# Optimization experiments

Measured on AMD Instinct MI355X. Metric: run time of the kernel, lower is better.

## Reference

```python
import jax, jax.numpy as jnp
import numpy as np

MP = 10242  # number of coarse (pooled) vertices = L.shape[0]


def setup_inputs() -> dict:
    key = jax.random.key(0)
    k1, k2, k3, k4 = jax.random.split(key, 4)
    B, M, F = 16, 40962, 128
    NNZ = 40968  # ~4 nonzeros per coarse vertex (barycentric pooling)
    x = jax.random.normal(k1, (B, M, F), dtype=jnp.float32)
    rows = jax.random.randint(k2, (NNZ,), 0, MP, dtype=jnp.int64)
    cols = jax.random.randint(k3, (NNZ,), 0, M, dtype=jnp.int64)
    vals = jax.random.uniform(k4, (NNZ,), dtype=jnp.float32)
    return {"x": x, "rows": rows, "cols": cols, "vals": vals}


def reference(x, rows, cols, vals):
    # Equivalent of tf.sparse_tensor_dense_matmul(L, reshape(transpose(x)))
    # L: sparse [Mp, M] in COO (rows, cols, vals); x: [B, M, F].
    # out[b, p, f] = sum_{k: rows[k]==p} vals[k] * x[b, cols[k], f]
    gathered = x[:, cols, :] * vals[None, :, None]          # [B, nnz, F]
    gathered = jnp.transpose(gathered, (1, 0, 2))           # [nnz, B, F]
    pooled = jax.ops.segment_sum(gathered, rows, num_segments=MP)  # [Mp, B, F]
    return jnp.transpose(pooled, (1, 0, 2))                 # [B, Mp, F]
```

## Files before the change

### kernel.cpp

```cpp
#include <hip/hip_runtime.h>

constexpr int MP  = 10242;
constexpr int B   = 16;
constexpr int M   = 40962;
constexpr int F   = 128;
constexpr int CAP = 32;

typedef float f32x4 __attribute__((ext_vector_type(4)));

__global__ void build_ell_kernel(const int* __restrict__ rows,
                                 const int* __restrict__ cols,
                                 const float* __restrict__ vals,
                                 int* __restrict__ counts,
                                 int2* __restrict__ ell,
                                 unsigned char* __restrict__ used,
                                 int nnz) {
    int k = blockIdx.x * blockDim.x + threadIdx.x;
    if (k < nnz) {
        int p = rows[k];
        int c = cols[k];
        if (used) used[c] = 1;
        int slot = atomicAdd(&counts[p], 1);
        if (slot < CAP) {
            ell[p * CAP + slot] = make_int2(c, __float_as_int(vals[k]));
        }
    }
}

__global__ __launch_bounds__(256)
void transpose_kernel(const float4* __restrict__ x,
                      const unsigned char* __restrict__ used,
                      float4* __restrict__ xt) {
    int m = blockIdx.x * 4 + (threadIdx.x >> 6);
    if (m >= M || !used[m]) return;
    int lane = threadIdx.x & 63;
    const float4* src = x + ((size_t)(lane >> 5) * M + (size_t)m) * 32 + (lane & 31);
    float4*       dst = xt + (size_t)m * 512 + lane;
    f32x4 v[8];
#pragma unroll
    for (int i = 0; i < 8; ++i)
        v[i] = __builtin_nontemporal_load((const f32x4*)(src + (size_t)(2 * i) * M * 32));
#pragma unroll
    for (int i = 0; i < 8; ++i)
        dst[i * 64] = *(float4*)&v[i];
}

__global__ __launch_bounds__(256)
void pool_xt_kernel(const float4* __restrict__ xt,
                    const int* __restrict__ counts,
                    const int2* __restrict__ ell,
                    float4* __restrict__ out) {
    const int p = blockIdx.x;
    const int t = threadIdx.x;
    int n = counts[p];
    n = n < CAP ? n : CAP;
    const int2* pe = ell + p * CAP;

    f32x4 acc0 = {0.f, 0.f, 0.f, 0.f}, acc1 = {0.f, 0.f, 0.f, 0.f};
    int j = 0;
    for (; j + 2 <= n; j += 2) {
        int2 e0 = pe[j], e1 = pe[j + 1];
        const f32x4* r0 = (const f32x4*)(xt + (size_t)e0.x * 512);
        const f32x4* r1 = (const f32x4*)(xt + (size_t)e1.x * 512);
        f32x4 a0 = r0[t], a1 = r0[t + 256];
        f32x4 b0 = r1[t], b1 = r1[t + 256];
        float v0 = __int_as_float(e0.y), v1 = __int_as_float(e1.y);
        acc0 += v0 * a0; acc1 += v0 * a1;
        acc0 += v1 * b0; acc1 += v1 * b1;
    }
    if (j < n) {
        int2 e = pe[j];
        const f32x4* r = (const f32x4*)(xt + (size_t)e.x * 512);
        float v = __int_as_float(e.y);
        acc0 += v * r[t]; acc1 += v * r[t + 256];
    }
    int b0i = t >> 5, l = t & 31;
    f32x4* o0 = (f32x4*)(out + ((size_t)b0i * MP + p) * 32 + l);
    f32x4* o1 = (f32x4*)(out + ((size_t)(b0i + 8) * MP + p) * 32 + l);
    __builtin_nontemporal_store(acc0, o0);
    __builtin_nontemporal_store(acc1, o1);
}

__global__ __launch_bounds__(256)
void pool_direct_kernel(const float4* __restrict__ x,
                        const int* __restrict__ counts,
                        const int2* __restrict__ ell,
                        float4* __restrict__ out) {
    const int p    = blockIdx.x;
    const int q    = threadIdx.x >> 6;
    const int lane = threadIdx.x & 63;
    const int bA   = (q << 1) | (lane >> 5);
    const int bB   = bA + 8;
    const int l    = lane & 31;

    int n = counts[p];
    n = n < CAP ? n : CAP;
    const int2* pe = ell + p * CAP;
    const float4* xA = x + (size_t)bA * (M * (F / 4));
    const float4* xB = x + (size_t)bB * (M * (F / 4));

    f32x4 accA = {0.f, 0.f, 0.f, 0.f}, accB = {0.f, 0.f, 0.f, 0.f};
    for (int j = 0; j < n; ++j) {
        int2 e = pe[j];
        float v = __int_as_float(e.y);
        f32x4 a = *(const f32x4*)&xA[(size_t)e.x * 32 + l];
        f32x4 c = *(const f32x4*)&xB[(size_t)e.x * 32 + l];
        accA += v * a;
        accB += v * c;
    }
    f32x4* oA = (f32x4*)(out + ((size_t)bA * MP + p) * 32 + l);
    f32x4* oB = (f32x4*)(out + ((size_t)bB * MP + p) * 32 + l);
    __builtin_nontemporal_store(accA, oA);
    __builtin_nontemporal_store(accB, oB);
}

extern "C" void kernel_launch(void* const* d_in, const int* in_sizes, int n_in,
                              void* d_out, int out_size, void* d_ws, size_t ws_size,
                              hipStream_t stream) {
    const float* x    = (const float*)d_in[0];
    const int*   rows = (const int*)d_in[1];
    const int*   cols = (const int*)d_in[2];
    const float* vals = (const float*)d_in[3];
    float* out = (float*)d_out;
    const int nnz = in_sizes[1];
    const int nb  = (nnz + 255) / 256;

    size_t xt_bytes   = (size_t)M * B * F * sizeof(float);
    size_t counts_off = xt_bytes;
    size_t ell_off    = counts_off + (size_t)MP * sizeof(int);
    size_t used_off   = ell_off + (size_t)MP * CAP * sizeof(int2);
    size_t needed     = used_off + (size_t)M;

    if (ws_size >= needed) {
        float* xt              = (float*)d_ws;
        int*   counts          = (int*)((char*)d_ws + counts_off);
        int2*  ell             = (int2*)((char*)d_ws + ell_off);
        unsigned char* used    = (unsigned char*)((char*)d_ws + used_off);

        hipMemsetAsync(counts, 0, MP * sizeof(int), stream);
        hipMemsetAsync(used, 0, M, stream);

        build_ell_kernel<<<nb, 256, 0, stream>>>(rows, cols, vals, counts, ell,
                                                 used, nnz);
        transpose_kernel<<<(M + 3) / 4, 256, 0, stream>>>((const float4*)x, used,
                                                          (float4*)xt);
        pool_xt_kernel<<<MP, 256, 0, stream>>>((const float4*)xt, counts, ell,
                                               (float4*)out);
    } else {
        int*  counts = (int*)d_ws;
        int2* ell    = (int2*)(counts + MP);
        hipMemsetAsync(counts, 0, MP * sizeof(int), stream);
        build_ell_kernel<<<nb, 256, 0, stream>>>(rows, cols, vals, counts, ell,
                                                 (unsigned char*)nullptr, nnz);
        pool_direct_kernel<<<MP, 256, 0, stream>>>((const float4*)x, counts, ell,
                                                   (float4*)out);
    }
}
```

Baseline: 524.7 us.

## Tile transpose through shared memory for contiguous reads and merge workspace memsets

The transpose kernel now handles 8 vertices per block, loading contiguous 4 KB runs of x per batch into shared memory and then writing each used vertex's 16x128 row block to xt. The goal is longer contiguous global reads than the old per-vertex 512-byte strided loads. The workspace is reordered so counts and the used-flag array sit next to each other and can be cleared with one memset, removing a launch. The cost is shared memory use and a block barrier, and blocks with sparse used flags still fetch some partial rows.

```diff
diff --git a/kernel.cpp b/kernel.cpp
--- a/kernel.cpp
+++ b/kernel.cpp
@@ -5,6 +5,7 @@
 constexpr int M   = 40962;
 constexpr int F   = 128;
 constexpr int CAP = 32;
+constexpr int TM  = 8;
 
 typedef float f32x4 __attribute__((ext_vector_type(4)));
 
@@ -31,18 +32,46 @@
 void transpose_kernel(const float4* __restrict__ x,
                       const unsigned char* __restrict__ used,
                       float4* __restrict__ xt) {
-    int m = blockIdx.x * 4 + (threadIdx.x >> 6);
-    if (m >= M || !used[m]) return;
-    int lane = threadIdx.x & 63;
-    const float4* src = x + ((size_t)(lane >> 5) * M + (size_t)m) * 32 + (lane & 31);
-    float4*       dst = xt + (size_t)m * 512 + lane;
-    f32x4 v[8];
+    __shared__ float4 tile[TM][B][F / 4];
+    const int m0   = blockIdx.x * TM;
+    const int t    = threadIdx.x;
+    const int w    = t >> 6;
+    const int lane = t & 63;
+
+    f32x4 v[16];
 #pragma unroll
-    for (int i = 0; i < 8; ++i)
-        v[i] = __builtin_nontemporal_load((const f32x4*)(src + (size_t)(2 * i) * M * 32));
+    for (int bi = 0; bi < 4; ++bi) {
+        int b = (w << 2) | bi;
+        const f32x4* src = (const f32x4*)(x + ((size_t)b * M + m0) * 32);
 #pragma unroll
-    for (int i = 0; i < 8; ++i)
-        dst[i * 64] = *(float4*)&v[i];
+        for (int jj = 0; jj < 4; ++jj) {
+            int idx = (jj << 6) | lane;
+            int gm  = m0 + (idx >> 5);
+            f32x4 tmp = {0.f, 0.f, 0.f, 0.f};
+            if (gm < M && used[gm]) tmp = src[idx];
+            v[(bi << 2) | jj] = tmp;
+        }
+    }
+#pragma unroll
+    for (int bi = 0; bi < 4; ++bi) {
+        int b = (w << 2) | bi;
+#pragma unroll
+        for (int jj = 0; jj < 4; ++jj) {
+            int idx = (jj << 6) | lane;
+            tile[idx >> 5][b][idx & 31] = *(float4*)&v[(bi << 2) | jj];
+        }
+    }
+    __syncthreads();
+#pragma unroll
+    for (int mm = 0; mm < TM; ++mm) {
+        int gm = m0 + mm;
+        if (gm < M && used[gm]) {
+            const float4* src = &tile[mm][0][0];
+            float4* dst = xt + (size_t)gm * 512;
+            dst[t]       = src[t];
+            dst[t + 256] = src[t + 256];
+        }
+    }
 }
 
 __global__ __launch_bounds__(256)
@@ -127,23 +156,22 @@
 
     size_t xt_bytes   = (size_t)M * B * F * sizeof(float);
     size_t counts_off = xt_bytes;
-    size_t ell_off    = counts_off + (size_t)MP * sizeof(int);
-    size_t used_off   = ell_off + (size_t)MP * CAP * sizeof(int2);
-    size_t needed     = used_off + (size_t)M;
+    size_t used_off   = counts_off + (size_t)MP * sizeof(int);
+    size_t ell_off    = (used_off + (size_t)M + 7) & ~(size_t)7;
+    size_t needed     = ell_off + (size_t)MP * CAP * sizeof(int2);
 
     if (ws_size >= needed) {
-        float* xt              = (float*)d_ws;
-        int*   counts          = (int*)((char*)d_ws + counts_off);
-        int2*  ell             = (int2*)((char*)d_ws + ell_off);
-        unsigned char* used    = (unsigned char*)((char*)d_ws + used_off);
+        float*         xt     = (float*)d_ws;
+        int*           counts = (int*)((char*)d_ws + counts_off);
+        unsigned char* used   = (unsigned char*)((char*)d_ws + used_off);
+        int2*          ell    = (int2*)((char*)d_ws + ell_off);
 
-        hipMemsetAsync(counts, 0, MP * sizeof(int), stream);
-        hipMemsetAsync(used, 0, M, stream);
+        hipMemsetAsync(counts, 0, (size_t)MP * sizeof(int) + (size_t)M, stream);
 
         build_ell_kernel<<<nb, 256, 0, stream>>>(rows, cols, vals, counts, ell,
                                                  used, nnz);
-        transpose_kernel<<<(M + 3) / 4, 256, 0, stream>>>((const float4*)x, used,
-                                                          (float4*)xt);
+        transpose_kernel<<<(M + TM - 1) / TM, 256, 0, stream>>>(
+            (const float4*)x, used, (float4*)xt);
         pool_xt_kernel<<<MP, 256, 0, stream>>>((const float4*)xt, counts, ell,
                                                (float4*)out);
     } else {
```

Result: slower. 616.9 us (+17.6%).
